# Kernel optimization log

Measured on AMD Instinct MI355X. Metric: run time of the kernel, lower is better.

The kernel has to match this reference:

```python
import jax, jax.numpy as jnp
import numpy as np

SEQ_LEN = 2048
DIM = 1024
DIM_HEAD = 64
NHEAD = DIM // DIM_HEAD


def setup_inputs() -> dict:
    key = jax.random.key(0)
    k1, k2, k3 = jax.random.split(key, 3)
    x = jax.random.normal(k1, (SEQ_LEN, DIM), dtype=jnp.float32)
    # ortho_init approximated by scaled gaussian weights (same math path in forward)
    Wqkv = jax.random.normal(k2, (DIM, 3 * DIM), dtype=jnp.float32) / np.sqrt(DIM)
    Wout = jax.random.normal(k3, (DIM, DIM), dtype=jnp.float32) / np.sqrt(DIM)
    bias = jnp.zeros((DIM,), dtype=jnp.float32)
    return {"x": x, "Wqkv": Wqkv, "Wout": Wout, "bias": bias}


def reference(x, Wqkv, Wout, bias):
    seq_len = x.shape[-2]
    qkv = x @ Wqkv  # [S, 3*dim]
    qkv = jnp.reshape(qkv, (-1, 3, NHEAD, DIM_HEAD))  # [S,3,H,D]
    qkv = jnp.swapaxes(qkv, 0, 2)  # [H,3,S,D]
    q, k, v = (jax.lax.index_in_dim(qkv, i, -3, keepdims=False) for i in range(3))
    # [H,S,S] full logits, scaled
    logits = q @ jnp.swapaxes(k, -1, -2) / jnp.sqrt(DIM_HEAD)
    mask = jnp.tril(jnp.ones((seq_len, seq_len), dtype=jnp.float32))
    logits = jnp.where(mask, logits, jnp.finfo(logits.dtype).min)
    dtype = logits.dtype
    probs = jax.nn.softmax(logits.astype(jnp.float32), axis=-1).astype(dtype)
    attn_outs = probs @ v  # [H,S,D]
    attn_outs = jnp.reshape(jnp.swapaxes(attn_outs, 0, 1), (-1, NHEAD * DIM_HEAD))
    return attn_outs @ Wout + bias
```

## Files before the change

### kernel.cpp

```cpp
#include <hip/hip_runtime.h>
#include <cstdint>

#define SEQ_LEN 2048
#define DIM 1024
#define NHEAD 16
#define DHEAD 64
#define QKV_LD (3 * DIM)

typedef unsigned short u16;
typedef short bf16x8 __attribute__((ext_vector_type(8)));
typedef float f32x4 __attribute__((ext_vector_type(4)));

__device__ __forceinline__ u16 f2bf(float f) {
    union { float f; unsigned u; } v;
    v.f = f;
    unsigned r = v.u + 0x7fff + ((v.u >> 16) & 1);
    return (u16)(r >> 16);
}

__device__ __forceinline__ void load_lds16(const void* g, void* l) {
    __builtin_amdgcn_global_load_lds(
        (const __attribute__((address_space(1))) void*)g,
        (__attribute__((address_space(3))) void*)l, 16, 0, 0);
}

__device__ __forceinline__ void transpose_tile(const float* __restrict__ W,
                                               u16* __restrict__ Wt, int K, int N,
                                               int bx, int by, int t, float (*tile)[33]) {
    const int n0 = bx * 32, k0 = by * 32;
    const int tx = t & 31, ty = t >> 5;
#pragma unroll
    for (int i = 0; i < 32; i += 8)
        tile[ty + i][tx] = W[(size_t)(k0 + ty + i) * N + n0 + tx];
    __syncthreads();
#pragma unroll
    for (int i = 0; i < 32; i += 8)
        Wt[(size_t)(n0 + ty + i) * K + k0 + tx] = f2bf(tile[tx][ty + i]);
}

__global__ __launch_bounds__(256) void prep_k(const float* __restrict__ x,
                                              const float* __restrict__ Wqkv,
                                              const float* __restrict__ Wout,
                                              u16* __restrict__ xb,
                                              u16* __restrict__ Wqkvt,
                                              u16* __restrict__ Woutt) {
    __shared__ float tile[32][33];
    const int b = blockIdx.x;
    const int t = threadIdx.x;
    if (b < 2048) {
        const int i = b * 256 + t;
        const float4 v = reinterpret_cast<const float4*>(x)[i];
        const unsigned p0 = (unsigned)f2bf(v.x) | ((unsigned)f2bf(v.y) << 16);
        const unsigned p1 = (unsigned)f2bf(v.z) | ((unsigned)f2bf(v.w) << 16);
        reinterpret_cast<uint2*>(xb)[i] = make_uint2(p0, p1);
    } else if (b < 5120) {
        const int b2 = b - 2048;
        transpose_tile(Wqkv, Wqkvt, DIM, QKV_LD, b2 % 96, b2 / 96, t, tile);
    } else {
        const int b3 = b - 5120;
        transpose_tile(Wout, Woutt, DIM, DIM, b3 & 31, b3 >> 5, t, tile);
    }
}

template <int MODE, int BM, int BN, int BK>
__global__ __launch_bounds__(256) void gemm_bf16(const u16* __restrict__ A,
                                                 const u16* __restrict__ Bt,
                                                 const float* __restrict__ bias,
                                                 void* __restrict__ Cout,
                                                 u16* __restrict__ kout,
                                                 u16* __restrict__ vout,
                                                 int M, int N, int K) {
    constexpr int AI = BM / 32;
    constexpr int BJ = BN / 32;
    constexpr int ASZ = BM * BK;
    constexpr int BSZ = BN * BK;
    __shared__ u16 As[2 * ASZ];
    __shared__ u16 Bs[2 * BSZ];

    const int t = threadIdx.x;
    const int lane = t & 63;
    const int quad = lane >> 4;
    const int l15 = lane & 15;
    const int w = t >> 6;
    const int wm = (w & 1) * (BM / 2);
    const int wn = (w >> 1) * (BN / 2);
    const int m0 = blockIdx.y * BM;
    const int n0 = blockIdx.x * BN;
    const int sr = t >> 2;
    const int sc = (t & 3) << 3;

    const u16* Ab = A + (size_t)(m0 + sr) * K + sc;
    const u16* Bb = Bt + (size_t)(n0 + sr) * K + sc;

    auto stage = [&](int buf, int k0) {
#pragma unroll
        for (int kc = 0; kc < BK / 32; ++kc) {
#pragma unroll
            for (int c = 0; c < BM / 64; ++c)
                load_lds16(Ab + (size_t)(c * 64) * K + k0 + kc * 32,
                           &As[buf * ASZ + kc * BM * 32 + c * 2048 + t * 8]);
#pragma unroll
            for (int c = 0; c < BN / 64; ++c)
                load_lds16(Bb + (size_t)(c * 64) * K + k0 + kc * 32,
                           &Bs[buf * BSZ + kc * BN * 32 + c * 2048 + t * 8]);
        }
    };

    stage(0, 0);
    f32x4 acc[AI][BJ] = {};

    const int niter = K / BK;
    for (int it = 0; it < niter; ++it) {
        const int cur = it & 1, nxt = cur ^ 1;
        __syncthreads();
        if (it + 1 < niter) stage(nxt, (it + 1) * BK);
#pragma unroll
        for (int kc = 0; kc < BK / 32; ++kc) {
            bf16x8 af[AI], bfr[BJ];
#pragma unroll
            for (int i = 0; i < AI; ++i)
                af[i] = *reinterpret_cast<const bf16x8*>(
                    &As[cur * ASZ + kc * BM * 32 + (wm + i * 16 + l15) * 32 + quad * 8]);
#pragma unroll
            for (int j = 0; j < BJ; ++j)
                bfr[j] = *reinterpret_cast<const bf16x8*>(
                    &Bs[cur * BSZ + kc * BN * 32 + (wn + j * 16 + l15) * 32 + quad * 8]);
#pragma unroll
            for (int i = 0; i < AI; ++i)
#pragma unroll
                for (int j = 0; j < BJ; ++j)
                    acc[i][j] =
                        __builtin_amdgcn_mfma_f32_16x16x32_bf16(af[i], bfr[j], acc[i][j], 0, 0, 0);
        }
    }

    if constexpr (MODE == 1) {
#pragma unroll
        for (int j = 0; j < BJ; ++j) {
            const int col = n0 + wn + j * 16 + l15;
            const float bv = bias[col];
#pragma unroll
            for (int i = 0; i < AI; ++i) {
                const int row = m0 + wm + i * 16 + quad * 4;
#pragma unroll
                for (int r = 0; r < 4; ++r)
                    ((float*)Cout)[(size_t)(row + r) * N + col] = acc[i][j][r] + bv;
            }
        }
    } else {
        const int region = n0 >> 10;
        if (region == 0) {
#pragma unroll
            for (int j = 0; j < BJ; ++j) {
                const int col = n0 + wn + j * 16 + l15;
#pragma unroll
                for (int i = 0; i < AI; ++i) {
                    const int row = m0 + wm + i * 16 + quad * 4;
#pragma unroll
                    for (int r = 0; r < 4; ++r)
                        ((u16*)Cout)[(size_t)(row + r) * DIM + col] = f2bf(acc[i][j][r]);
                }
            }
        } else if (region == 1) {
#pragma unroll
            for (int j = 0; j < BJ; ++j) {
                const int hd = n0 + wn + j * 16 + l15 - 1024;
                const int d = hd & 63, hb = hd & ~63;
#pragma unroll
                for (int i = 0; i < AI; ++i) {
                    const int row = m0 + wm + i * 16 + quad * 4;
#pragma unroll
                    for (int r = 0; r < 4; ++r) {
                        const int s = row + r;
                        const int pos = hb + ((((d >> 3) ^ (s & 7)) << 3) | (d & 7));
                        kout[(size_t)s * DIM + pos] = f2bf(acc[i][j][r]);
                    }
                }
            }
        } else {
#pragma unroll
            for (int j = 0; j < BJ; ++j) {
                const int hd = n0 + wn + j * 16 + l15 - 2048;
#pragma unroll
                for (int i = 0; i < AI; ++i) {
                    const int srow = m0 + wm + i * 16 + quad * 4;
                    const unsigned p0 = (unsigned)f2bf(acc[i][j][0]) |
                                        ((unsigned)f2bf(acc[i][j][1]) << 16);
                    const unsigned p1 = (unsigned)f2bf(acc[i][j][2]) |
                                        ((unsigned)f2bf(acc[i][j][3]) << 16);
                    const int pos = (srow & ~63) + ((((srow >> 3) & 7) ^ (hd & 7)) << 3) +
                                    (srow & 7);
                    *reinterpret_cast<uint2*>(&vout[(size_t)hd * SEQ_LEN + pos]) =
                        make_uint2(p0, p1);
                }
            }
        }
    }
}

__global__ __launch_bounds__(256) void attn_mfma(const u16* __restrict__ Qb,
                                                 const u16* __restrict__ Kb,
                                                 const u16* __restrict__ Vg,
                                                 u16* __restrict__ O) {
    constexpr int PSTR = 40;
    __shared__ u16 SM[4096 + 8192 + 8192 + 4 * 32 * PSTR];
    u16* Qs = SM;
    u16* Ks = SM + 4096;
    u16* Vs = SM + 4096 + 8192;
    u16* Ps = SM + 4096 + 16384;
    float* OredF = (float*)SM;
    float* LredF = (float*)(SM + 4096 + 8192 + 4096);

    const int b = blockIdx.x;
    const int hb = b >> 4;
    const int qt = (hb < 16) ? (31 - hb) : (hb - 16);
    const int h = b & 15;
    const int q0 = qt * 64;

    const int t = threadIdx.x;
    const int lane = t & 63;
    const int quad = lane >> 4;
    const int l15 = lane & 15;
    const int w = t >> 6;
    const int wq = w >> 1;
    const int wk = w & 1;

    const int drow = t >> 3;
    const int doff = (t & 7) * 8;

    auto stageK = [&](int buf, int j0) {
#pragma unroll
        for (int c = 0; c < 2; ++c)
            load_lds16(Kb + (size_t)(j0 + c * 32 + drow) * DIM + h * DHEAD + doff,
                       &Ks[buf * 4096 + c * 2048 + t * 8]);
    };
    auto stageV = [&](int buf, int j0) {
#pragma unroll
        for (int c = 0; c < 2; ++c)
            load_lds16(Vg + (size_t)(h * DHEAD + c * 32 + drow) * SEQ_LEN + j0 + doff,
                       &Vs[buf * 4096 + c * 2048 + t * 8]);
    };

#pragma unroll
    for (int c = 0; c < 2; ++c)
        load_lds16(Qb + (size_t)(q0 + c * 32 + drow) * DIM + h * DHEAD + doff,
                   &Qs[c * 2048 + t * 8]);
    stageK(0, 0);
    stageV(0, 0);
    __syncthreads();

    bf16x8 qf[2][2];
#pragma unroll
    for (int qq = 0; qq < 2; ++qq)
#pragma unroll
        for (int dc = 0; dc < 2; ++dc)
            qf[qq][dc] = *reinterpret_cast<const bf16x8*>(
                &Qs[(wq * 32 + qq * 16 + l15) * 64 + dc * 32 + quad * 8]);

    f32x4 oacc[2][4] = {};
    float lsum[2][4] = {};
    u16* Pw = Ps + w * 32 * PSTR;
    constexpr float SCL = 0.18033688f;

    for (int jt = 0; jt <= qt; ++jt) {
        const int cur = jt & 1, nxt = cur ^ 1;
        if (jt > 0) __syncthreads();
        if (jt < qt) {
            stageK(nxt, (jt + 1) * 64);
            stageV(nxt, (jt + 1) * 64);
        }

        f32x4 sacc[2][2] = {};
#pragma unroll
        for (int nn = 0; nn < 2; ++nn)
#pragma unroll
            for (int dc = 0; dc < 2; ++dc) {
                const bf16x8 kf = *reinterpret_cast<const bf16x8*>(
                    &Ks[cur * 4096 + (wk * 32 + nn * 16 + l15) * 64 +
                        (((dc * 4 + quad) ^ (l15 & 7)) << 3)]);
#pragma unroll
                for (int qq = 0; qq < 2; ++qq)
                    sacc[qq][nn] =
                        __builtin_amdgcn_mfma_f32_16x16x32_bf16(qf[qq][dc], kf, sacc[qq][nn], 0, 0, 0);
            }

        const bool diag = (jt == qt);
#pragma unroll
        for (int qq = 0; qq < 2; ++qq)
#pragma unroll
            for (int r = 0; r < 4; ++r) {
                const int rowl = wq * 32 + qq * 16 + quad * 4 + r;
                float p0 = sacc[qq][0][r] * SCL, p1 = sacc[qq][1][r] * SCL;
                if (diag) {
                    if (wk * 32 + l15 > rowl) p0 = -1e30f;
                    if (wk * 32 + 16 + l15 > rowl) p1 = -1e30f;
                }
                p0 = exp2f(p0);
                p1 = exp2f(p1);
                lsum[qq][r] += p0 + p1;
                const int pr = (qq * 16 + quad * 4 + r) * PSTR;
                Pw[pr + l15] = (u16)(__float_as_uint(p0) >> 16);
                Pw[pr + 16 + l15] = (u16)(__float_as_uint(p1) >> 16);
            }

#pragma unroll
        for (int qq = 0; qq < 2; ++qq) {
            const bf16x8 pf =
                *reinterpret_cast<const bf16x8*>(&Pw[(qq * 16 + l15) * PSTR + quad * 8]);
#pragma unroll
            for (int nd = 0; nd < 4; ++nd) {
                const bf16x8 vf = *reinterpret_cast<const bf16x8*>(
                    &Vs[cur * 4096 + (nd * 16 + l15) * 64 +
                        (((wk * 4 + quad) ^ (l15 & 7)) << 3)]);
                oacc[qq][nd] =
                    __builtin_amdgcn_mfma_f32_16x16x32_bf16(pf, vf, oacc[qq][nd], 0, 0, 0);
            }
        }
    }

#pragma unroll
    for (int qq = 0; qq < 2; ++qq)
#pragma unroll
        for (int r = 0; r < 4; ++r) {
            float l = lsum[qq][r];
#pragma unroll
            for (int off = 1; off < 16; off <<= 1) l += __shfl_xor(l, off, 64);
            lsum[qq][r] = l;
        }
    __syncthreads();
    if (wk == 1) {
#pragma unroll
        for (int qq = 0; qq < 2; ++qq)
#pragma unroll
            for (int r = 0; r < 4; ++r) {
                const int rowl = wq * 32 + qq * 16 + quad * 4 + r;
                if (l15 == 0) LredF[rowl] = lsum[qq][r];
#pragma unroll
                for (int nd = 0; nd < 4; ++nd)
                    OredF[rowl * 68 + nd * 16 + l15] = oacc[qq][nd][r];
            }
    }
    __syncthreads();
    if (wk == 0) {
#pragma unroll
        for (int qq = 0; qq < 2; ++qq)
#pragma unroll
            for (int r = 0; r < 4; ++r) {
                const int rowl = wq * 32 + qq * 16 + quad * 4 + r;
                const float inv = 1.0f / (lsum[qq][r] + LredF[rowl]);
                const int row = q0 + rowl;
#pragma unroll
                for (int nd = 0; nd < 4; ++nd)
                    O[(size_t)row * DIM + h * DHEAD + nd * 16 + l15] =
                        f2bf((oacc[qq][nd][r] + OredF[rowl * 68 + nd * 16 + l15]) * inv);
            }
    }
}

extern "C" void kernel_launch(void* const* d_in, const int* in_sizes, int n_in,
                              void* d_out, int out_size, void* d_ws, size_t ws_size,
                              hipStream_t stream) {
    const float* x = (const float*)d_in[0];
    const float* Wqkv = (const float*)d_in[1];
    const float* Wout = (const float*)d_in[2];
    const float* bias = (const float*)d_in[3];
    float* out = (float*)d_out;

    char* ws = (char*)d_ws;
    u16* xb = (u16*)ws;
    u16* Wqkvt = (u16*)(ws + (4u << 20));
    u16* Woutt = (u16*)(ws + (10u << 20));
    u16* Qb = (u16*)(ws + (12u << 20));
    u16* Kb = (u16*)(ws + (16u << 20));
    u16* Vg = (u16*)(ws + (20u << 20));
    u16* Ob = (u16*)(ws + (24u << 20));

    prep_k<<<dim3(6144), 256, 0, stream>>>(x, Wqkv, Wout, xb, Wqkvt, Woutt);

    gemm_bf16<0, 128, 64, 64><<<dim3(QKV_LD / 64, SEQ_LEN / 128), 256, 0, stream>>>(
        xb, Wqkvt, nullptr, Qb, Kb, Vg, SEQ_LEN, QKV_LD, DIM);

    attn_mfma<<<dim3(32 * NHEAD), 256, 0, stream>>>(Qb, Kb, Vg, Ob);

    gemm_bf16<1, 64, 64, 64><<<dim3(DIM / 64, SEQ_LEN / 64), 256, 0, stream>>>(
        Ob, Woutt, bias, out, nullptr, nullptr, SEQ_LEN, DIM, DIM);
}
```

Before: 140.5 us.

## Halve attention query tile to 32 rows and fold softmax scale into Q projection

The attention kernel now processes 32 query rows per block instead of 64, doubling the grid to 1024 blocks with a new four-group ordering that pairs long and short causal tiles. LDS use shrinks because Q is staged once into a region the P buffer then reuses. The softmax scale multiply moves from the inner attention loop into the QKV GEMM epilogue, where Q is scaled before bf16 rounding. This is meant to improve occupancy and load balance across CUs, at the cost of re-reading K/V twice as often and doing half the MFMA work per K/V tile load.

```diff
diff --git a/kernel.cpp b/kernel.cpp
--- a/kernel.cpp
+++ b/kernel.cpp
@@ -150,6 +150,7 @@
     } else {
         const int region = n0 >> 10;
         if (region == 0) {
+            constexpr float SCL = 0.18033688f;
 #pragma unroll
             for (int j = 0; j < BJ; ++j) {
                 const int col = n0 + wn + j * 16 + l15;
@@ -158,7 +159,7 @@
                     const int row = m0 + wm + i * 16 + quad * 4;
 #pragma unroll
                     for (int r = 0; r < 4; ++r)
-                        ((u16*)Cout)[(size_t)(row + r) * DIM + col] = f2bf(acc[i][j][r]);
+                        ((u16*)Cout)[(size_t)(row + r) * DIM + col] = f2bf(acc[i][j][r] * SCL);
                 }
             }
         } else if (region == 1) {
@@ -202,20 +203,21 @@
                                                  const u16* __restrict__ Kb,
                                                  const u16* __restrict__ Vg,
                                                  u16* __restrict__ O) {
-    constexpr int PSTR = 40;
-    __shared__ u16 SM[4096 + 8192 + 8192 + 4 * 32 * PSTR];
-    u16* Qs = SM;
-    u16* Ks = SM + 4096;
-    u16* Vs = SM + 4096 + 8192;
-    u16* Ps = SM + 4096 + 16384;
+    constexpr int PSTR = 36;
+    __shared__ u16 SM[2304 + 8192 + 8192];
+    u16* Ps = SM;
+    u16* Ks = SM + 2304;
+    u16* Vs = SM + 2304 + 8192;
     float* OredF = (float*)SM;
-    float* LredF = (float*)(SM + 4096 + 8192 + 4096);
+    float* LredF = (float*)(SM + 4608);
 
     const int b = blockIdx.x;
+    const int h = b & 15;
     const int hb = b >> 4;
-    const int qt = (hb < 16) ? (31 - hb) : (hb - 16);
-    const int h = b & 15;
-    const int q0 = qt * 64;
+    const int g = hb >> 4, ii = hb & 15;
+    const int qt = (g == 0) ? (63 - ii) : (g == 1) ? (32 + ii) : (g == 2) ? (31 - ii) : ii;
+    const int q0 = qt * 32;
+    const int jmax = qt >> 1;
 
     const int t = threadIdx.x;
     const int lane = t & 63;
@@ -241,36 +243,31 @@
                        &Vs[buf * 4096 + c * 2048 + t * 8]);
     };
 
-#pragma unroll
-    for (int c = 0; c < 2; ++c)
-        load_lds16(Qb + (size_t)(q0 + c * 32 + drow) * DIM + h * DHEAD + doff,
-                   &Qs[c * 2048 + t * 8]);
+    load_lds16(Qb + (size_t)(q0 + drow) * DIM + h * DHEAD + doff, &SM[t * 8]);
     stageK(0, 0);
     stageV(0, 0);
     __syncthreads();
 
-    bf16x8 qf[2][2];
-#pragma unroll
-    for (int qq = 0; qq < 2; ++qq)
-#pragma unroll
-        for (int dc = 0; dc < 2; ++dc)
-            qf[qq][dc] = *reinterpret_cast<const bf16x8*>(
-                &Qs[(wq * 32 + qq * 16 + l15) * 64 + dc * 32 + quad * 8]);
-
-    f32x4 oacc[2][4] = {};
-    float lsum[2][4] = {};
-    u16* Pw = Ps + w * 32 * PSTR;
-    constexpr float SCL = 0.18033688f;
-
-    for (int jt = 0; jt <= qt; ++jt) {
+    bf16x8 qf[2];
+#pragma unroll
+    for (int dc = 0; dc < 2; ++dc)
+        qf[dc] = *reinterpret_cast<const bf16x8*>(
+            &SM[(wq * 16 + l15) * 64 + dc * 32 + quad * 8]);
+    __syncthreads();
+
+    f32x4 oacc[4] = {};
+    float lsum[4] = {};
+    u16* Pw = Ps + w * 16 * PSTR;
+
+    for (int jt = 0; jt <= jmax; ++jt) {
         const int cur = jt & 1, nxt = cur ^ 1;
         if (jt > 0) __syncthreads();
-        if (jt < qt) {
+        if (jt < jmax) {
             stageK(nxt, (jt + 1) * 64);
             stageV(nxt, (jt + 1) * 64);
         }
 
-        f32x4 sacc[2][2] = {};
+        f32x4 sacc[2] = {};
 #pragma unroll
         for (int nn = 0; nn < 2; ++nn)
 #pragma unroll
@@ -278,82 +275,67 @@
                 const bf16x8 kf = *reinterpret_cast<const bf16x8*>(
                     &Ks[cur * 4096 + (wk * 32 + nn * 16 + l15) * 64 +
                         (((dc * 4 + quad) ^ (l15 & 7)) << 3)]);
-#pragma unroll
-                for (int qq = 0; qq < 2; ++qq)
-                    sacc[qq][nn] =
-                        __builtin_amdgcn_mfma_f32_16x16x32_bf16(qf[qq][dc], kf, sacc[qq][nn], 0, 0, 0);
-            }
-
-        const bool diag = (jt == qt);
-#pragma unroll
-        for (int qq = 0; qq < 2; ++qq)
-#pragma unroll
-            for (int r = 0; r < 4; ++r) {
-                const int rowl = wq * 32 + qq * 16 + quad * 4 + r;
-                float p0 = sacc[qq][0][r] * SCL, p1 = sacc[qq][1][r] * SCL;
-                if (diag) {
-                    if (wk * 32 + l15 > rowl) p0 = -1e30f;
-                    if (wk * 32 + 16 + l15 > rowl) p1 = -1e30f;
-                }
-                p0 = exp2f(p0);
-                p1 = exp2f(p1);
-                lsum[qq][r] += p0 + p1;
-                const int pr = (qq * 16 + quad * 4 + r) * PSTR;
-                Pw[pr + l15] = (u16)(__float_as_uint(p0) >> 16);
-                Pw[pr + 16 + l15] = (u16)(__float_as_uint(p1) >> 16);
-            }
-
-#pragma unroll
-        for (int qq = 0; qq < 2; ++qq) {
-            const bf16x8 pf =
-                *reinterpret_cast<const bf16x8*>(&Pw[(qq * 16 + l15) * PSTR + quad * 8]);
-#pragma unroll
-            for (int nd = 0; nd < 4; ++nd) {
-                const bf16x8 vf = *reinterpret_cast<const bf16x8*>(
-                    &Vs[cur * 4096 + (nd * 16 + l15) * 64 +
-                        (((wk * 4 + quad) ^ (l15 & 7)) << 3)]);
-                oacc[qq][nd] =
-                    __builtin_amdgcn_mfma_f32_16x16x32_bf16(pf, vf, oacc[qq][nd], 0, 0, 0);
-            }
-        }
-    }
-
-#pragma unroll
-    for (int qq = 0; qq < 2; ++qq)
+                sacc[nn] = __builtin_amdgcn_mfma_f32_16x16x32_bf16(qf[dc], kf, sacc[nn], 0, 0, 0);
+            }
+
+        const bool diag = (jt == jmax);
 #pragma unroll
         for (int r = 0; r < 4; ++r) {
-            float l = lsum[qq][r];
-#pragma unroll
-            for (int off = 1; off < 16; off <<= 1) l += __shfl_xor(l, off, 64);
-            lsum[qq][r] = l;
-        }
+            const int rowl = wq * 16 + quad * 4 + r;
+            float p0 = sacc[0][r], p1 = sacc[1][r];
+            if (diag) {
+                const int rowi = ((qt & 1) << 5) + rowl;
+                if (wk * 32 + l15 > rowi) p0 = -1e30f;
+                if (wk * 32 + 16 + l15 > rowi) p1 = -1e30f;
+            }
+            p0 = exp2f(p0);
+            p1 = exp2f(p1);
+            lsum[r] += p0 + p1;
+            const int pr = (quad * 4 + r) * PSTR;
+            Pw[pr + l15] = (u16)(__float_as_uint(p0) >> 16);
+            Pw[pr + 16 + l15] = (u16)(__float_as_uint(p1) >> 16);
+        }
+
+        const bf16x8 pf = *reinterpret_cast<const bf16x8*>(&Pw[l15 * PSTR + quad * 8]);
+#pragma unroll
+        for (int nd = 0; nd < 4; ++nd) {
+            const bf16x8 vf = *reinterpret_cast<const bf16x8*>(
+                &Vs[cur * 4096 + (nd * 16 + l15) * 64 +
+                    (((wk * 4 + quad) ^ (l15 & 7)) << 3)]);
+            oacc[nd] = __builtin_amdgcn_mfma_f32_16x16x32_bf16(pf, vf, oacc[nd], 0, 0, 0);
+        }
+    }
+
+#pragma unroll
+    for (int r = 0; r < 4; ++r) {
+        float l = lsum[r];
+#pragma unroll
+        for (int off = 1; off < 16; off <<= 1) l += __shfl_xor(l, off, 64);
+        lsum[r] = l;
+    }
     __syncthreads();
     if (wk == 1) {
 #pragma unroll
-        for (int qq = 0; qq < 2; ++qq)
-#pragma unroll
-            for (int r = 0; r < 4; ++r) {
-                const int rowl = wq * 32 + qq * 16 + quad * 4 + r;
-                if (l15 == 0) LredF[rowl] = lsum[qq][r];
-#pragma unroll
-                for (int nd = 0; nd < 4; ++nd)
-                    OredF[rowl * 68 + nd * 16 + l15] = oacc[qq][nd][r];
-            }
+        for (int r = 0; r < 4; ++r) {
+            const int rowl = wq * 16 + quad * 4 + r;
+            if (l15 == 0) LredF[rowl] = lsum[r];
+#pragma unroll
+            for (int nd = 0; nd < 4; ++nd)
+                OredF[rowl * 68 + nd * 16 + l15] = oacc[nd][r];
+        }
     }
     __syncthreads();
     if (wk == 0) {
 #pragma unroll
-        for (int qq = 0; qq < 2; ++qq)
-#pragma unroll
-            for (int r = 0; r < 4; ++r) {
-                const int rowl = wq * 32 + qq * 16 + quad * 4 + r;
-                const float inv = 1.0f / (lsum[qq][r] + LredF[rowl]);
-                const int row = q0 + rowl;
-#pragma unroll
-                for (int nd = 0; nd < 4; ++nd)
-                    O[(size_t)row * DIM + h * DHEAD + nd * 16 + l15] =
-                        f2bf((oacc[qq][nd][r] + OredF[rowl * 68 + nd * 16 + l15]) * inv);
-            }
+        for (int r = 0; r < 4; ++r) {
+            const int rowl = wq * 16 + quad * 4 + r;
+            const float inv = 1.0f / (lsum[r] + LredF[rowl]);
+            const int row = q0 + rowl;
+#pragma unroll
+            for (int nd = 0; nd < 4; ++nd)
+                O[(size_t)row * DIM + h * DHEAD + nd * 16 + l15] =
+                    f2bf((oacc[nd][r] + OredF[rowl * 68 + nd * 16 + l15]) * inv);
+        }
     }
 }
 
@@ -380,7 +362,7 @@
     gemm_bf16<0, 128, 64, 64><<<dim3(QKV_LD / 64, SEQ_LEN / 128), 256, 0, stream>>>(
         xb, Wqkvt, nullptr, Qb, Kb, Vg, SEQ_LEN, QKV_LD, DIM);
 
-    attn_mfma<<<dim3(32 * NHEAD), 256, 0, stream>>>(Qb, Kb, Vg, Ob);
+    attn_mfma<<<dim3(64 * NHEAD), 256, 0, stream>>>(Qb, Kb, Vg, Ob);
 
     gemm_bf16<1, 64, 64, 64><<<dim3(DIM / 64, SEQ_LEN / 64), 256, 0, stream>>>(
         Ob, Woutt, bias, out, nullptr, nullptr, SEQ_LEN, DIM, DIM);
```

Measured after the change: 141.6 us. Within noise of the previous version (+0.8%).
